# Kernel tuning notes

Hardware: AMD Instinct MI355X
Metric: run time of the kernel (lower is better)

## Reference

```python
import jax, jax.numpy as jnp
import numpy as np

B, L, DIM, H = 1, 2048, 1536, 24
HD = DIM // H  # head_dim = 64
EPS = 1e-6


def _rmsnorm(x, g):
    # RMSNorm over last dim with learnable scale (matches RMSNorm with elementwise_affine=True)
    return x * jax.lax.rsqrt(jnp.mean(x * x, axis=-1, keepdims=True) + EPS) * g


def setup_inputs() -> dict:
    key = jax.random.key(0)
    ks = jax.random.split(key, 4)
    s = 0.02
    return {
        "x": jax.random.normal(ks[0], (B, L, DIM), jnp.float32),
        "w_qkv": jax.random.normal(ks[1], (3 * DIM, DIM), jnp.float32) * s,
        "b_qkv": jnp.zeros((3 * DIM,), jnp.float32),
        "w_proj": jax.random.normal(ks[2], (DIM, DIM), jnp.float32) * s,
        "b_proj": jnp.zeros((DIM,), jnp.float32),
        "g_q": jnp.ones((HD,), jnp.float32),
        "g_k": jnp.ones((HD,), jnp.float32),
    }


def reference(x, w_qkv, b_qkv, w_proj, b_proj, g_q, g_k):
    Bb, Ll, C = x.shape
    # fused QKV projection: [B,L,C] -> [B,L,3C] -> [B,L,3,H,HD]
    qkv = (x @ w_qkv.T + b_qkv).reshape(Bb, Ll, 3, H, HD)
    q, k, v = qkv[:, :, 0], qkv[:, :, 1], qkv[:, :, 2]  # each [B,L,H,HD]
    # per-head RMS norm on q/k (qk_norm='rms')
    q = _rmsnorm(q, g_q)
    k = _rmsnorm(k, g_k)
    # scaled dot-product attention (torch SDPA default scale = 1/sqrt(head_dim))
    scale = 1.0 / np.sqrt(HD).astype(np.float32)
    scores = jnp.einsum('bqhd,bkhd->bhqk', q, k) * scale  # [B,H,L,L]
    attn = jax.nn.softmax(scores, axis=-1)
    o = jnp.einsum('bhqk,bkhd->bqhd', attn, v).reshape(Bb, Ll, C)
    # output projection
    return o @ w_proj.T + b_proj
```

## Files before the change

### kernel.cpp

```cpp
#include <hip/hip_runtime.h>
#include <stdint.h>

#define L_SEQ 2048
#define DIM 1536
#define NH 24
#define HD 64
#define NQKV 4608

typedef unsigned short u16;
typedef __attribute__((ext_vector_type(4))) float f32x4;
typedef __attribute__((ext_vector_type(8))) short bf16x8;
typedef __attribute__((ext_vector_type(4))) u16 u16x4;
typedef __attribute__((ext_vector_type(8))) u16 u16x8;

__device__ __forceinline__ u16 f2bf(float f) {
  unsigned u = __builtin_bit_cast(unsigned, f);
  u += 0x7fffu + ((u >> 16) & 1u);
  return (u16)(u >> 16);
}
__device__ __forceinline__ float b2f(u16 u) {
  return __builtin_bit_cast(float, (unsigned)u << 16);
}
__device__ __forceinline__ unsigned cvt_pk_bf16(float lo, float hi) {
  unsigned r;
  asm("v_cvt_pk_bf16_f32 %0, %1, %2" : "=v"(r) : "v"(lo), "v"(hi));
  return r;
}

__device__ __forceinline__ void gload_lds16(const void* g, void* lds) {
  __builtin_amdgcn_global_load_lds(
      (const __attribute__((address_space(1))) unsigned int*)g,
      (__attribute__((address_space(3))) unsigned int*)lds, 16, 0, 0);
}

__global__ __launch_bounds__(256) void cast3_kernel(const float* __restrict__ x,
                                                    const float* __restrict__ wq,
                                                    const float* __restrict__ wp,
                                                    u16* __restrict__ out) {
  const int n1 = (L_SEQ * DIM) / 4;
  const int n2 = (NQKV * DIM) / 4;
  const int n3 = (DIM * DIM) / 4;
  const int tot = n1 + n2 + n3;
  for (int i = blockIdx.x * 256 + threadIdx.x; i < tot; i += gridDim.x * 256) {
    const f32x4* src;
    int j;
    if (i < n1) {
      src = (const f32x4*)x;
      j = i;
    } else if (i < n1 + n2) {
      src = (const f32x4*)wq;
      j = i - n1;
    } else {
      src = (const f32x4*)wp;
      j = i - n1 - n2;
    }
    f32x4 v = src[j];
    u16x4 o;
    o.x = f2bf(v.x);
    o.y = f2bf(v.y);
    o.z = f2bf(v.z);
    o.w = f2bf(v.w);
    ((u16x4*)out)[i] = o;
  }
}

template <int WRITE_BF16>
__global__ __launch_bounds__(256) void gemm_bt(const u16* __restrict__ A,
                                               const u16* __restrict__ B,
                                               const float* __restrict__ bias,
                                               void* __restrict__ Cout,
                                               int M, int N, int K) {
  __shared__ u16 As[2][128 * 32];
  __shared__ u16 Bs[2][128 * 32];
  const int mb = M >> 7;
  const int f = (int)blockIdx.x;
  const int f2 = (f & 7) * ((int)gridDim.x >> 3) + (f >> 3);
  const int bx = f2 / mb;
  const int by = f2 % mb;
  const int tid = threadIdx.x;
  const int lane = tid & 63;
  const int wv = tid >> 6;
  const int wr = wv >> 1, wc = wv & 1;

  f32x4 acc[4][4];
#pragma unroll
  for (int i = 0; i < 4; i++)
#pragma unroll
    for (int j = 0; j < 4; j++) acc[i][j] = (f32x4)(0.0f);

  const int e0 = tid * 8;
  const int r0 = e0 >> 5, c0 = e0 & 31;
  const u16* Ag0 = A + (size_t)(by * 128 + r0) * K + c0;
  const u16* Ag1 = A + (size_t)(by * 128 + r0 + 64) * K + c0;
  const u16* Bg0 = B + (size_t)(bx * 128 + r0) * K + c0;
  const u16* Bg1 = B + (size_t)(bx * 128 + r0 + 64) * K + c0;
  const int kc = (lane >> 4) * 8;
  const int wb = wv * 1024;

  gload_lds16(Ag0, (char*)As[0] + wb);
  gload_lds16(Ag1, (char*)As[0] + wb + 4096);
  gload_lds16(Bg0, (char*)Bs[0] + wb);
  gload_lds16(Bg1, (char*)Bs[0] + wb + 4096);
  __syncthreads();

  int cur = 0;
  for (int k0 = 0; k0 < K; k0 += 32) {
    const int nxt = cur ^ 1;
    if (k0 + 32 < K) {
      gload_lds16(Ag0 + k0 + 32, (char*)As[nxt] + wb);
      gload_lds16(Ag1 + k0 + 32, (char*)As[nxt] + wb + 4096);
      gload_lds16(Bg0 + k0 + 32, (char*)Bs[nxt] + wb);
      gload_lds16(Bg1 + k0 + 32, (char*)Bs[nxt] + wb + 4096);
    }
    const u16* Asc = As[cur];
    const u16* Bsc = Bs[cur];
    bf16x8 af[4], bfr[4];
#pragma unroll
    for (int mt = 0; mt < 4; mt++)
      af[mt] = *(const bf16x8*)&Asc[(wr * 64 + mt * 16 + (lane & 15)) * 32 + kc];
#pragma unroll
    for (int nt = 0; nt < 4; nt++)
      bfr[nt] = *(const bf16x8*)&Bsc[(wc * 64 + nt * 16 + (lane & 15)) * 32 + kc];
#pragma unroll
    for (int mt = 0; mt < 4; mt++)
#pragma unroll
      for (int nt = 0; nt < 4; nt++)
        acc[mt][nt] = __builtin_amdgcn_mfma_f32_16x16x32_bf16(af[mt], bfr[nt],
                                                              acc[mt][nt], 0, 0, 0);
    __syncthreads();
    cur = nxt;
  }

  const int colb = bx * 128 + wc * 64 + (lane & 15);
  const int rowb = by * 128 + wr * 64 + ((lane >> 4) << 2);
#pragma unroll
  for (int nt = 0; nt < 4; nt++) {
    const int col = colb + nt * 16;
    const float bv = bias[col];
#pragma unroll
    for (int mt = 0; mt < 4; mt++) {
#pragma unroll
      for (int r = 0; r < 4; r++) {
        const int row = rowb + mt * 16 + r;
        float v = acc[mt][nt][r] + bv;
        if (WRITE_BF16)
          ((u16*)Cout)[(size_t)row * N + col] = f2bf(v);
        else
          ((float*)Cout)[(size_t)row * N + col] = v;
      }
    }
  }
}

__global__ __launch_bounds__(256) void qkvnorm_kernel(const u16* __restrict__ qkv,
                                                      const float* __restrict__ gq,
                                                      const float* __restrict__ gk,
                                                      u16* __restrict__ Qh,
                                                      u16* __restrict__ Kh,
                                                      u16* __restrict__ Vt) {
  const int h = blockIdx.y;
  const int lblk = blockIdx.x * 64;
  const int tid = threadIdx.x;
  const int lane = tid & 63, wv = tid >> 6;
  __shared__ u16 vt[64][64];
  const float gqv = gq[lane] * 0.125f * 1.44269504088896f;
  const float gkv = gk[lane];
#pragma unroll 1
  for (int i = 0; i < 16; i++) {
    const int l = lblk + wv * 16 + i;
    const size_t base = (size_t)l * NQKV + h * HD + lane;
    const float q = b2f(qkv[base]);
    const float k = b2f(qkv[base + DIM]);
    float sq = q * q, sk = k * k;
#pragma unroll
    for (int m = 32; m; m >>= 1) {
      sq += __shfl_xor(sq, m);
      sk += __shfl_xor(sk, m);
    }
    const float rq = rsqrtf(sq * (1.0f / 64.0f) + 1e-6f);
    const float rk = rsqrtf(sk * (1.0f / 64.0f) + 1e-6f);
    const size_t ho = ((size_t)h * L_SEQ + l) * HD + lane;
    Qh[ho] = f2bf(q * rq * gqv);
    Kh[ho] = f2bf(k * rk * gkv);
    vt[wv * 16 + i][lane] = qkv[base + 2 * DIM];
  }
  __syncthreads();
  const int d = tid >> 2;
  const int cb = (tid & 3) * 16;
  u16* dst = Vt + ((size_t)h * HD + d) * L_SEQ + lblk + cb;
#pragma unroll
  for (int j0 = 0; j0 < 4; j0++) {
    u16x4 o;
    o.x = vt[cb + j0 * 4 + 0][d];
    o.y = vt[cb + j0 * 4 + 1][d];
    o.z = vt[cb + j0 * 4 + 2][d];
    o.w = vt[cb + j0 * 4 + 3][d];
    *(u16x4*)(dst + j0 * 4) = o;
  }
}

__global__ __launch_bounds__(256) void flash_kernel(const u16* __restrict__ Qh,
                                                    const u16* __restrict__ Kh,
                                                    const u16* __restrict__ Vt,
                                                    u16* __restrict__ O) {
  const int f = (int)blockIdx.y * (L_SEQ / 64) + (int)blockIdx.x;
  const int f2 = (f & 7) * 96 + (f >> 3);
  const int h = f2 >> 5;
  const int qblk = (f2 & 31) * 64;
  const int tid = threadIdx.x;
  const int lane = tid & 63, wv = tid >> 6;
  __shared__ u16 Ks[64][64];
  __shared__ u16 Vs[64][64];
  __shared__ u16 Ps[4][16][64];

  const int l4 = lane & 15;
  const int g = lane >> 4;
  const int kc = g * 8;
  const int swz = (l4 & 7) << 3;

  const int qrow = qblk + wv * 16 + l4;
  const u16* Qp = Qh + ((size_t)h * L_SEQ + qrow) * HD;
  const bf16x8 qf0 = *(const bf16x8*)(Qp + kc);
  const bf16x8 qf1 = *(const bf16x8*)(Qp + 32 + kc);
  const bf16x8 ones = (bf16x8)(short)0x3F80;

  f32x4 oacc[4];
#pragma unroll
  for (int dt = 0; dt < 4; dt++) oacc[dt] = (f32x4)(0.0f);
  float mr = -1e30f;
  float lr[4] = {0.f, 0.f, 0.f, 0.f};

  const int krow = tid >> 3;
  const int kcol = (tid & 7) * 8;
  const u16* Kg = Kh + (size_t)h * L_SEQ * HD + (size_t)krow * HD + kcol;
  u16* KsW0 = &Ks[krow][kcol ^ ((krow & 7) << 3)];
  u16* KsW1 = KsW0 + 32 * 64;
  const int vd = tid >> 2;
  const int vcol = (tid & 3) * 16;
  const u16* Vg = Vt + ((size_t)h * HD + vd) * L_SEQ;
  u16* VsW0 = &Vs[vd][vcol ^ ((vd & 7) << 3)];
  u16* VsW1 = &Vs[vd][(vcol + 8) ^ ((vd & 7) << 3)];

  bf16x8 kr0 = *(const bf16x8*)(Kg);
  bf16x8 kr1 = *(const bf16x8*)(Kg + 32 * HD);
  bf16x8 vr0 = *(const bf16x8*)(Vg + vcol);
  bf16x8 vr1 = *(const bf16x8*)(Vg + vcol + 8);

  for (int kb = 0; kb < L_SEQ; kb += 64) {
    __syncthreads();
    *(bf16x8*)KsW0 = kr0;
    *(bf16x8*)KsW1 = kr1;
    *(bf16x8*)VsW0 = vr0;
    *(bf16x8*)VsW1 = vr1;
    if (kb + 64 < L_SEQ) {
      kr0 = *(const bf16x8*)(Kg + (size_t)(kb + 64) * HD);
      kr1 = *(const bf16x8*)(Kg + (size_t)(kb + 96) * HD);
      vr0 = *(const bf16x8*)(Vg + kb + 64 + vcol);
      vr1 = *(const bf16x8*)(Vg + kb + 72 + vcol);
    }
    __syncthreads();

    f32x4 s[4];
    __builtin_amdgcn_s_setprio(1);
#pragma unroll
    for (int st = 0; st < 4; st++) {
      const u16* kp = &Ks[st * 16 + l4][0];
      bf16x8 ka = *(const bf16x8*)(kp + (kc ^ swz));
      bf16x8 kb2 = *(const bf16x8*)(kp + ((kc + 32) ^ swz));
      s[st] = __builtin_amdgcn_mfma_f32_16x16x32_bf16(ka, qf0, (f32x4)(0.0f), 0, 0, 0);
      s[st] = __builtin_amdgcn_mfma_f32_16x16x32_bf16(kb2, qf1, s[st], 0, 0, 0);
    }
    __builtin_amdgcn_s_setprio(0);

    float mx = fmaxf(fmaxf(s[0][0], s[0][1]), fmaxf(s[0][2], s[0][3]));
    mx = fmaxf(fmaxf(mx, s[1][0]), fmaxf(s[1][1], s[1][2]));
    mx = fmaxf(fmaxf(mx, s[1][3]), fmaxf(s[2][0], s[2][1]));
    mx = fmaxf(fmaxf(mx, s[2][2]), fmaxf(s[2][3], s[3][0]));
    mx = fmaxf(fmaxf(mx, s[3][1]), fmaxf(s[3][2], s[3][3]));
    mx = fmaxf(mx, __shfl_xor(mx, 16));
    mx = fmaxf(mx, __shfl_xor(mx, 32));

    if (__any(mx > mr + 8.0f)) {
      const float nm = fmaxf(mr, mx);
      const float sclo = __builtin_amdgcn_exp2f(mr - nm);
      mr = nm;
      float scl[4];
#pragma unroll
      for (int r = 0; r < 4; r++) scl[r] = __shfl(sclo, g * 4 + r);
#pragma unroll
      for (int r = 0; r < 4; r++) lr[r] *= scl[r];
#pragma unroll
      for (int dt = 0; dt < 4; dt++)
#pragma unroll
        for (int r = 0; r < 4; r++) oacc[dt][r] *= scl[r];
    }

    u16* pr = &Ps[wv][l4][0];
#pragma unroll
    for (int st = 0; st < 4; st++) {
      uint2 pw;
      pw.x = cvt_pk_bf16(__builtin_amdgcn_exp2f(s[st][0] - mr),
                         __builtin_amdgcn_exp2f(s[st][1] - mr));
      pw.y = cvt_pk_bf16(__builtin_amdgcn_exp2f(s[st][2] - mr),
                         __builtin_amdgcn_exp2f(s[st][3] - mr));
      *(uint2*)(pr + ((st * 16 + g * 4) ^ swz)) = pw;
    }

    const u16* pp = &Ps[wv][l4][0];
    bf16x8 pf0 = *(const bf16x8*)(pp + (kc ^ swz));
    bf16x8 pf1 = *(const bf16x8*)(pp + ((kc + 32) ^ swz));
    __builtin_amdgcn_s_setprio(1);
    f32x4 ls = __builtin_amdgcn_mfma_f32_16x16x32_bf16(pf0, ones, (f32x4)(0.0f), 0, 0, 0);
    ls = __builtin_amdgcn_mfma_f32_16x16x32_bf16(pf1, ones, ls, 0, 0, 0);
#pragma unroll
    for (int dt = 0; dt < 4; dt++) {
      const u16* vp = &Vs[dt * 16 + l4][0];
      bf16x8 vf0 = *(const bf16x8*)(vp + (kc ^ swz));
      bf16x8 vf1 = *(const bf16x8*)(vp + ((kc + 32) ^ swz));
      oacc[dt] = __builtin_amdgcn_mfma_f32_16x16x32_bf16(pf0, vf0, oacc[dt], 0, 0, 0);
      oacc[dt] = __builtin_amdgcn_mfma_f32_16x16x32_bf16(pf1, vf1, oacc[dt], 0, 0, 0);
    }
    __builtin_amdgcn_s_setprio(0);
#pragma unroll
    for (int r = 0; r < 4; r++) lr[r] += ls[r];
  }

#pragma unroll
  for (int r = 0; r < 4; r++) {
    const float inv = 1.0f / lr[r];
    const int row = qblk + wv * 16 + g * 4 + r;
#pragma unroll
    for (int dt = 0; dt < 4; dt++) {
      const int col = h * HD + dt * 16 + l4;
      O[(size_t)row * DIM + col] = f2bf(oacc[dt][r] * inv);
    }
  }
}

extern "C" void kernel_launch(void* const* d_in, const int* in_sizes, int n_in,
                              void* d_out, int out_size, void* d_ws, size_t ws_size,
                              hipStream_t stream) {
  const float* x = (const float*)d_in[0];
  const float* w_qkv = (const float*)d_in[1];
  const float* b_qkv = (const float*)d_in[2];
  const float* w_proj = (const float*)d_in[3];
  const float* b_proj = (const float*)d_in[4];
  const float* g_q = (const float*)d_in[5];
  const float* g_k = (const float*)d_in[6];

  char* ws = (char*)d_ws;
  u16* x_b = (u16*)(ws + 0);
  u16* wqkv_b = (u16*)(ws + 6291456);
  u16* wpj_b = (u16*)(ws + 20447232);
  u16* qkv = (u16*)(ws + 25165824);
  u16* Qh = (u16*)(ws + 44040192);
  u16* Kh = (u16*)(ws + 50331648);
  u16* Vt = (u16*)(ws + 56623104);
  u16* Ob = (u16*)(ws + 62914560);

  cast3_kernel<<<3072, 256, 0, stream>>>(x, w_qkv, w_proj, x_b);

  gemm_bt<1><<<(L_SEQ / 128) * (NQKV / 128), 256, 0, stream>>>(
      x_b, wqkv_b, b_qkv, (void*)qkv, L_SEQ, NQKV, DIM);

  qkvnorm_kernel<<<dim3(L_SEQ / 64, NH), 256, 0, stream>>>(qkv, g_q, g_k, Qh, Kh, Vt);

  flash_kernel<<<dim3(L_SEQ / 64, NH), 256, 0, stream>>>(Qh, Kh, Vt, Ob);

  gemm_bt<0><<<(L_SEQ / 128) * (DIM / 128), 256, 0, stream>>>(
      Ob, wpj_b, b_proj, d_out, L_SEQ, DIM, DIM);
}
```

Before: 153.2 us.

## Fuse QK RMSNorm and V transpose into QKV GEMM epilogue

Removes the separate qkvnorm kernel and the intermediate bf16 qkv buffer. The QKV GEMM epilogue now computes the per-head RMS norm for Q and K with shuffle reductions across the 16 lanes holding a row's 64 columns, and writes V directly in transposed layout. This saves one launch and a full write and read of the qkv tensor. In exchange the epilogue does more work and its stores are scattered 2-byte writes.

```diff
diff --git a/kernel.cpp b/kernel.cpp
--- a/kernel.cpp
+++ b/kernel.cpp
@@ -64,11 +64,16 @@
   }
 }
 
-template <int WRITE_BF16>
+template <int MODE>
 __global__ __launch_bounds__(256) void gemm_bt(const u16* __restrict__ A,
                                                const u16* __restrict__ B,
                                                const float* __restrict__ bias,
                                                void* __restrict__ Cout,
+                                               const float* __restrict__ gq,
+                                               const float* __restrict__ gk,
+                                               u16* __restrict__ Qh,
+                                               u16* __restrict__ Kh,
+                                               u16* __restrict__ Vt,
                                                int M, int N, int K) {
   __shared__ u16 As[2][128 * 32];
   __shared__ u16 Bs[2][128 * 32];
@@ -79,6 +84,7 @@
   const int by = f2 % mb;
   const int tid = threadIdx.x;
   const int lane = tid & 63;
+  const int l4 = lane & 15;
   const int wv = tid >> 6;
   const int wr = wv >> 1, wc = wv & 1;
 
@@ -117,10 +123,10 @@
     bf16x8 af[4], bfr[4];
 #pragma unroll
     for (int mt = 0; mt < 4; mt++)
-      af[mt] = *(const bf16x8*)&Asc[(wr * 64 + mt * 16 + (lane & 15)) * 32 + kc];
+      af[mt] = *(const bf16x8*)&Asc[(wr * 64 + mt * 16 + l4) * 32 + kc];
 #pragma unroll
     for (int nt = 0; nt < 4; nt++)
-      bfr[nt] = *(const bf16x8*)&Bsc[(wc * 64 + nt * 16 + (lane & 15)) * 32 + kc];
+      bfr[nt] = *(const bf16x8*)&Bsc[(wc * 64 + nt * 16 + l4) * 32 + kc];
 #pragma unroll
     for (int mt = 0; mt < 4; mt++)
 #pragma unroll
@@ -131,71 +137,74 @@
     cur = nxt;
   }
 
-  const int colb = bx * 128 + wc * 64 + (lane & 15);
-  const int rowb = by * 128 + wr * 64 + ((lane >> 4) << 2);
-#pragma unroll
-  for (int nt = 0; nt < 4; nt++) {
-    const int col = colb + nt * 16;
-    const float bv = bias[col];
-#pragma unroll
-    for (int mt = 0; mt < 4; mt++) {
-#pragma unroll
-      for (int r = 0; r < 4; r++) {
-        const int row = rowb + mt * 16 + r;
-        float v = acc[mt][nt][r] + bv;
-        if (WRITE_BF16)
-          ((u16*)Cout)[(size_t)row * N + col] = f2bf(v);
-        else
-          ((float*)Cout)[(size_t)row * N + col] = v;
+  const int l0 = by * 128 + wr * 64 + ((lane >> 4) << 2);
+  if (MODE == 0) {
+    const int colb = bx * 128 + wc * 64 + l4;
+#pragma unroll
+    for (int nt = 0; nt < 4; nt++) {
+      const int col = colb + nt * 16;
+      const float bv = bias[col];
+#pragma unroll
+      for (int mt = 0; mt < 4; mt++) {
+#pragma unroll
+        for (int r = 0; r < 4; r++) {
+          const int row = l0 + mt * 16 + r;
+          ((float*)Cout)[(size_t)row * N + col] = acc[mt][nt][r] + bv;
+        }
       }
     }
-  }
-}
-
-__global__ __launch_bounds__(256) void qkvnorm_kernel(const u16* __restrict__ qkv,
-                                                      const float* __restrict__ gq,
-                                                      const float* __restrict__ gk,
-                                                      u16* __restrict__ Qh,
-                                                      u16* __restrict__ Kh,
-                                                      u16* __restrict__ Vt) {
-  const int h = blockIdx.y;
-  const int lblk = blockIdx.x * 64;
-  const int tid = threadIdx.x;
-  const int lane = tid & 63, wv = tid >> 6;
-  __shared__ u16 vt[64][64];
-  const float gqv = gq[lane] * 0.125f * 1.44269504088896f;
-  const float gkv = gk[lane];
-#pragma unroll 1
-  for (int i = 0; i < 16; i++) {
-    const int l = lblk + wv * 16 + i;
-    const size_t base = (size_t)l * NQKV + h * HD + lane;
-    const float q = b2f(qkv[base]);
-    const float k = b2f(qkv[base + DIM]);
-    float sq = q * q, sk = k * k;
-#pragma unroll
-    for (int m = 32; m; m >>= 1) {
-      sq += __shfl_xor(sq, m);
-      sk += __shfl_xor(sk, m);
-    }
-    const float rq = rsqrtf(sq * (1.0f / 64.0f) + 1e-6f);
-    const float rk = rsqrtf(sk * (1.0f / 64.0f) + 1e-6f);
-    const size_t ho = ((size_t)h * L_SEQ + l) * HD + lane;
-    Qh[ho] = f2bf(q * rq * gqv);
-    Kh[ho] = f2bf(k * rk * gkv);
-    vt[wv * 16 + i][lane] = qkv[base + 2 * DIM];
-  }
-  __syncthreads();
-  const int d = tid >> 2;
-  const int cb = (tid & 3) * 16;
-  u16* dst = Vt + ((size_t)h * HD + d) * L_SEQ + lblk + cb;
-#pragma unroll
-  for (int j0 = 0; j0 < 4; j0++) {
-    u16x4 o;
-    o.x = vt[cb + j0 * 4 + 0][d];
-    o.y = vt[cb + j0 * 4 + 1][d];
-    o.z = vt[cb + j0 * 4 + 2][d];
-    o.w = vt[cb + j0 * 4 + 3][d];
-    *(u16x4*)(dst + j0 * 4) = o;
+  } else {
+    const int colbase = bx * 128 + wc * 64;
+    const int sector = colbase / DIM;
+    const int h = (colbase % DIM) >> 6;
+    if (sector == 2) {
+#pragma unroll
+      for (int nt = 0; nt < 4; nt++) {
+        const int d = nt * 16 + l4;
+        const float bv = bias[colbase + d];
+        u16* dst = Vt + ((size_t)h * HD + d) * L_SEQ;
+#pragma unroll
+        for (int mt = 0; mt < 4; mt++) {
+          u16x4 o;
+          o.x = f2bf(acc[mt][nt][0] + bv);
+          o.y = f2bf(acc[mt][nt][1] + bv);
+          o.z = f2bf(acc[mt][nt][2] + bv);
+          o.w = f2bf(acc[mt][nt][3] + bv);
+          *(u16x4*)(dst + l0 + mt * 16) = o;
+        }
+      }
+    } else {
+      u16* Out = (sector == 0) ? Qh : Kh;
+      float gv[4], bv[4];
+#pragma unroll
+      for (int nt = 0; nt < 4; nt++) {
+        const int d = nt * 16 + l4;
+        bv[nt] = bias[colbase + d];
+        gv[nt] = (sector == 0) ? gq[d] * (0.125f * 1.44269504088896f) : gk[d];
+      }
+#pragma unroll
+      for (int mt = 0; mt < 4; mt++) {
+#pragma unroll
+        for (int r = 0; r < 4; r++) {
+          const float v0 = acc[mt][0][r] + bv[0];
+          const float v1 = acc[mt][1][r] + bv[1];
+          const float v2 = acc[mt][2][r] + bv[2];
+          const float v3 = acc[mt][3][r] + bv[3];
+          float ssq = v0 * v0 + v1 * v1 + v2 * v2 + v3 * v3;
+          ssq += __shfl_xor(ssq, 1);
+          ssq += __shfl_xor(ssq, 2);
+          ssq += __shfl_xor(ssq, 4);
+          ssq += __shfl_xor(ssq, 8);
+          const float rn = rsqrtf(ssq * (1.0f / 64.0f) + 1e-6f);
+          const int row = l0 + mt * 16 + r;
+          u16* op = Out + ((size_t)h * L_SEQ + row) * HD + l4;
+          op[0] = f2bf(v0 * rn * gv[0]);
+          op[16] = f2bf(v1 * rn * gv[1]);
+          op[32] = f2bf(v2 * rn * gv[2]);
+          op[48] = f2bf(v3 * rn * gv[3]);
+        }
+      }
+    }
   }
 }
 
@@ -352,21 +361,19 @@
   u16* x_b = (u16*)(ws + 0);
   u16* wqkv_b = (u16*)(ws + 6291456);
   u16* wpj_b = (u16*)(ws + 20447232);
-  u16* qkv = (u16*)(ws + 25165824);
-  u16* Qh = (u16*)(ws + 44040192);
-  u16* Kh = (u16*)(ws + 50331648);
-  u16* Vt = (u16*)(ws + 56623104);
-  u16* Ob = (u16*)(ws + 62914560);
+  u16* Qh = (u16*)(ws + 25165824);
+  u16* Kh = (u16*)(ws + 31457280);
+  u16* Vt = (u16*)(ws + 37748736);
+  u16* Ob = (u16*)(ws + 44040192);
 
   cast3_kernel<<<3072, 256, 0, stream>>>(x, w_qkv, w_proj, x_b);
 
-  gemm_bt<1><<<(L_SEQ / 128) * (NQKV / 128), 256, 0, stream>>>(
-      x_b, wqkv_b, b_qkv, (void*)qkv, L_SEQ, NQKV, DIM);
-
-  qkvnorm_kernel<<<dim3(L_SEQ / 64, NH), 256, 0, stream>>>(qkv, g_q, g_k, Qh, Kh, Vt);
+  gemm_bt<2><<<(L_SEQ / 128) * (NQKV / 128), 256, 0, stream>>>(
+      x_b, wqkv_b, b_qkv, nullptr, g_q, g_k, Qh, Kh, Vt, L_SEQ, NQKV, DIM);
 
   flash_kernel<<<dim3(L_SEQ / 64, NH), 256, 0, stream>>>(Qh, Kh, Vt, Ob);
 
   gemm_bt<0><<<(L_SEQ / 128) * (DIM / 128), 256, 0, stream>>>(
-      Ob, wpj_b, b_proj, d_out, L_SEQ, DIM, DIM);
-}
+      Ob, wpj_b, b_proj, d_out, nullptr, nullptr, nullptr, nullptr, nullptr,
+      L_SEQ, DIM, DIM);
+}
```

New measurement: 166.0 us. 1.08x slower.
